# Performance work log

Hardware: AMD Instinct MI355X
Metric: run time of the kernel (lower is better)

## Reference

```python
import jax, jax.numpy as jnp
import numpy as np

B, S, H, A = 64, 4096, 256, 128


def entmax15(z):
    # exact entmax-1.5 along the last axis (Peters & Martins 2019)
    z = z / 2.0
    z = z - jnp.max(z, axis=-1, keepdims=True)
    zs = -jnp.sort(-z, axis=-1)                      # descending sort
    n = zs.shape[-1]
    k = jnp.arange(1, n + 1, dtype=z.dtype)
    mean = jnp.cumsum(zs, axis=-1) / k
    mean_sq = jnp.cumsum(zs * zs, axis=-1) / k
    ss = k * (mean_sq - mean * mean)
    delta = jnp.clip((1.0 - ss) / k, 0.0)
    tau = mean - jnp.sqrt(delta)
    k_star = jnp.sum(tau <= zs, axis=-1)             # support size per row
    tau_star = jnp.take_along_axis(tau, (k_star - 1)[..., None], axis=-1)
    return jnp.square(jnp.clip(z - tau_star, 0.0))


def setup_inputs() -> dict:
    key = jax.random.key(0)
    k0, k1, k2, k3, k4 = jax.random.split(key, 5)
    lim1 = 1.0 / np.sqrt(H)
    lim2 = 1.0 / np.sqrt(A)
    return {
        "lstm_output": jax.random.normal(k0, (B, S, H), dtype=jnp.float32),
        "W1": jax.random.uniform(k1, (H, A), jnp.float32, -lim1, lim1),
        "b1": jax.random.uniform(k2, (A,), jnp.float32, -lim1, lim1),
        "W2": jax.random.uniform(k3, (A, 1), jnp.float32, -lim2, lim2),
        "b2": jax.random.uniform(k4, (1,), jnp.float32, -lim2, lim2),
    }


def reference(lstm_output, W1, b1, W2, b2):
    # score MLP: Linear -> Tanh -> Linear -> squeeze(-1)  => [B, S]
    h = jnp.tanh(jnp.einsum("bsh,ha->bsa", lstm_output, W1) + b1)
    scores = (jnp.einsum("bsa,ao->bso", h, W2) + b2)[..., 0]
    weights = entmax15(scores)                       # entmax over seq axis (dim=1)
    context = jnp.einsum("bsh,bs->bh", lstm_output, weights)
    return (context, weights)
```

## Files before the change

### kernel.cpp

```cpp
#include <hip/hip_runtime.h>
#include <hip/hip_bf16.h>

#define BB 64
#define SS 4096
#define HH 256
#define AA 128
#define MT 128
#define BK 64
#define XST 72

typedef _Float16 half4v __attribute__((ext_vector_type(4)));
typedef _Float16 half8v __attribute__((ext_vector_type(8)));
typedef float floatx16 __attribute__((ext_vector_type(16)));

__device__ __forceinline__ float fast_tanh(float x) {
    float xc = fminf(fmaxf(x, -9.0f), 9.0f);
    float e = __expf(2.0f * xc);
    return 1.0f - __fdividef(2.0f, e + 1.0f);
}

__global__ void convert_w1(const float* __restrict__ W1, _Float16* __restrict__ Wt) {
    int n = blockIdx.x;
    int k = threadIdx.x;
    Wt[n * HH + k] = (_Float16)W1[k * AA + n];
}

__global__ __launch_bounds__(256) void score_mfma(
    const float* __restrict__ X,
    const _Float16* __restrict__ Wt,
    const float* __restrict__ b1,
    const float* __restrict__ W2,
    const float* __restrict__ b2,
    float* __restrict__ scores)
{
    __shared__ float smem_f[9216];
    _Float16* Xs = (_Float16*)smem_f;
    _Float16* Ws = (_Float16*)smem_f + MT * XST;
    float* part = smem_f;

    const int tid   = threadIdx.x;
    const int m0    = blockIdx.x * MT;
    const int wid   = tid >> 6;
    const int lane  = tid & 63;
    const int lrow  = lane & 31;
    const int lhalf = lane >> 5;
    const int wr    = (wid & 1) * 64;
    const int wc    = (wid >> 1) * 64;

    floatx16 acc[2][2];
    #pragma unroll
    for (int i = 0; i < 2; ++i)
        #pragma unroll
        for (int j = 0; j < 2; ++j)
            #pragma unroll
            for (int r = 0; r < 16; ++r) acc[i][j][r] = 0.0f;

    for (int k0 = 0; k0 < HH; k0 += BK) {
        #pragma unroll
        for (int p = 0; p < 8; ++p) {
            int idx = tid + p * 256;
            int row = idx >> 4, c4 = idx & 15;
            float4 v = *(const float4*)(X + (size_t)(m0 + row) * HH + k0 + c4 * 4);
            half4v hv;
            hv[0] = (_Float16)v.x; hv[1] = (_Float16)v.y;
            hv[2] = (_Float16)v.z; hv[3] = (_Float16)v.w;
            *(half4v*)(Xs + row * XST + c4 * 4) = hv;
        }
        #pragma unroll
        for (int p = 0; p < 4; ++p) {
            int idx = tid + p * 256;
            int n = idx >> 3, u = idx & 7;
            uint4 v = *(const uint4*)(Wt + (size_t)n * HH + k0 + u * 8);
            *(uint4*)(Ws + n * XST + u * 8) = v;
        }
        __syncthreads();
        #pragma unroll
        for (int kk = 0; kk < BK; kk += 16) {
            half8v a0 = *(half8v*)(Xs + (wr + lrow) * XST + kk + lhalf * 8);
            half8v a1 = *(half8v*)(Xs + (wr + 32 + lrow) * XST + kk + lhalf * 8);
            half8v b0 = *(half8v*)(Ws + (wc + lrow) * XST + kk + lhalf * 8);
            half8v bq = *(half8v*)(Ws + (wc + 32 + lrow) * XST + kk + lhalf * 8);
            acc[0][0] = __builtin_amdgcn_mfma_f32_32x32x16_f16(a0, b0, acc[0][0], 0, 0, 0);
            acc[0][1] = __builtin_amdgcn_mfma_f32_32x32x16_f16(a0, bq, acc[0][1], 0, 0, 0);
            acc[1][0] = __builtin_amdgcn_mfma_f32_32x32x16_f16(a1, b0, acc[1][0], 0, 0, 0);
            acc[1][1] = __builtin_amdgcn_mfma_f32_32x32x16_f16(a1, bq, acc[1][1], 0, 0, 0);
        }
        __syncthreads();
    }

    const int cA = wc + lrow;
    const int cB = wc + 32 + lrow;
    const float b1A = b1[cA], b1B = b1[cB];
    const float w2A = W2[cA], w2B = W2[cB];
    #pragma unroll
    for (int i = 0; i < 2; ++i) {
        #pragma unroll
        for (int r = 0; r < 16; ++r) {
            float hA = fast_tanh(acc[i][0][r] + b1A) * w2A;
            float hB = fast_tanh(acc[i][1][r] + b1B) * w2B;
            int row = wr + i * 32 + (r & 3) + 8 * (r >> 2) + 4 * lhalf;
            part[row * 65 + (wid >> 1) * 32 + lrow] = hA + hB;
        }
    }
    __syncthreads();
    if (tid < MT) {
        float s = b2[0];
        #pragma unroll
        for (int c = 0; c < 64; ++c) s += part[tid * 65 + c];
        scores[m0 + tid] = s;
    }
}

__global__ __launch_bounds__(256) void entmax_kernel(
    float* __restrict__ buf, float* __restrict__ ctx)
{
    __shared__ float sred[4];
    const int b = blockIdx.x, tid = threadIdx.x;
    float* p = buf + (size_t)b * SS;

    float z[16];
    #pragma unroll
    for (int j = 0; j < 16; ++j) z[j] = p[tid + j * 256] * 0.5f;

    float m = -1e30f;
    #pragma unroll
    for (int j = 0; j < 16; ++j) m = fmaxf(m, z[j]);
    #pragma unroll
    for (int o = 1; o < 64; o <<= 1) m = fmaxf(m, __shfl_xor(m, o));
    if ((tid & 63) == 0) sred[tid >> 6] = m;
    __syncthreads();
    m = fmaxf(fmaxf(sred[0], sred[1]), fmaxf(sred[2], sred[3]));
    __syncthreads();
    #pragma unroll
    for (int j = 0; j < 16; ++j) z[j] -= m;

    float lo = -1.0f, hi = 0.0f;
    for (int it = 0; it < 35; ++it) {
        float tau = 0.5f * (lo + hi);
        float s = 0.0f;
        #pragma unroll
        for (int j = 0; j < 16; ++j) {
            float d = fmaxf(z[j] - tau, 0.0f);
            s = fmaf(d, d, s);
        }
        #pragma unroll
        for (int o = 1; o < 64; o <<= 1) s += __shfl_xor(s, o);
        if ((tid & 63) == 0) sred[tid >> 6] = s;
        __syncthreads();
        s = sred[0] + sred[1] + sred[2] + sred[3];
        __syncthreads();
        if (s >= 1.0f) lo = tau; else hi = tau;
    }
    const float tau = 0.5f * (lo + hi);

    #pragma unroll
    for (int j = 0; j < 16; ++j) {
        float d = fmaxf(z[j] - tau, 0.0f);
        p[tid + j * 256] = d * d;
    }
    ctx[b * HH + tid] = 0.0f;
}

__global__ __launch_bounds__(256) void context_kernel(
    const float* __restrict__ X, const float* __restrict__ w,
    float* __restrict__ ctx)
{
    const int b  = blockIdx.y;
    const int s0 = blockIdx.x * 128;
    const int h  = threadIdx.x;

    __shared__ float ws_[128];
    __shared__ int nzflag;
    if (h == 0) nzflag = 0;
    __syncthreads();
    if (h < 128) {
        float v = w[(size_t)b * SS + s0 + h];
        ws_[h] = v;
        if (v > 0.0f) nzflag = 1;
    }
    __syncthreads();
    if (!nzflag) return;

    float acc = 0.0f;
    const float* xp = X + ((size_t)b * SS + s0) * HH + h;
    #pragma unroll 4
    for (int i = 0; i < 128; ++i) {
        float wv = ws_[i];
        if (wv != 0.0f) acc = fmaf(xp[(size_t)i * HH], wv, acc);
    }
    atomicAdd(&ctx[b * HH + h], acc);
}

extern "C" void kernel_launch(void* const* d_in, const int* in_sizes, int n_in,
                              void* d_out, int out_size, void* d_ws, size_t ws_size,
                              hipStream_t stream) {
    const float* X  = (const float*)d_in[0];
    const float* W1 = (const float*)d_in[1];
    const float* b1 = (const float*)d_in[2];
    const float* W2 = (const float*)d_in[3];
    const float* b2 = (const float*)d_in[4];

    float* out = (float*)d_out;
    float* ctx = out;
    float* wts = out + BB * HH;
    _Float16* Wt = (_Float16*)d_ws;

    convert_w1<<<AA, HH, 0, stream>>>(W1, Wt);
    score_mfma<<<(BB * SS) / MT, 256, 0, stream>>>(X, Wt, b1, W2, b2, wts);
    entmax_kernel<<<BB, 256, 0, stream>>>(wts, ctx);
    context_kernel<<<dim3(SS / 128, BB), 256, 0, stream>>>(X, wts, ctx);
}
```

Measured before the change: 401.4 us.

## Stream X directly into MFMA registers without LDS staging per wave

The score GEMM no longer stages X and W tiles in shared memory behind block barriers. Each wave now owns 32 rows and the full 128-column output, loading X rows straight from global memory into fp16 MFMA operands and reading W fragments from global memory (L2/L1 cached). The second linear layer is reduced with wave shuffles instead of an LDS partial-sum buffer. This removes the LDS traffic and __syncthreads, at the cost of repeated, uncoalesced global loads of W per wave and less load coalescing for X.

```diff
diff --git a/kernel.cpp b/kernel.cpp
--- a/kernel.cpp
+++ b/kernel.cpp
@@ -5,11 +5,7 @@
 #define SS 4096
 #define HH 256
 #define AA 128
-#define MT 128
-#define BK 64
-#define XST 72
 
-typedef _Float16 half4v __attribute__((ext_vector_type(4)));
 typedef _Float16 half8v __attribute__((ext_vector_type(8)));
 typedef float floatx16 __attribute__((ext_vector_type(16)));
 
@@ -25,7 +21,7 @@
     Wt[n * HH + k] = (_Float16)W1[k * AA + n];
 }
 
-__global__ __launch_bounds__(256) void score_mfma(
+__global__ __launch_bounds__(256) void score_stream(
     const float* __restrict__ X,
     const _Float16* __restrict__ Wt,
     const float* __restrict__ b1,
@@ -33,81 +29,59 @@
     const float* __restrict__ b2,
     float* __restrict__ scores)
 {
-    __shared__ float smem_f[9216];
-    _Float16* Xs = (_Float16*)smem_f;
-    _Float16* Ws = (_Float16*)smem_f + MT * XST;
-    float* part = smem_f;
-
     const int tid   = threadIdx.x;
-    const int m0    = blockIdx.x * MT;
     const int wid   = tid >> 6;
     const int lane  = tid & 63;
     const int lrow  = lane & 31;
     const int lhalf = lane >> 5;
-    const int wr    = (wid & 1) * 64;
-    const int wc    = (wid >> 1) * 64;
+    const int m0    = blockIdx.x * 128 + wid * 32;
 
-    floatx16 acc[2][2];
+    const float* xp = X + (size_t)(m0 + lrow) * HH + lhalf * 8;
+
+    floatx16 acc[4];
     #pragma unroll
-    for (int i = 0; i < 2; ++i)
+    for (int nt = 0; nt < 4; ++nt)
         #pragma unroll
-        for (int j = 0; j < 2; ++j)
-            #pragma unroll
-            for (int r = 0; r < 16; ++r) acc[i][j][r] = 0.0f;
+        for (int r = 0; r < 16; ++r) acc[nt][r] = 0.0f;
 
-    for (int k0 = 0; k0 < HH; k0 += BK) {
+    #pragma unroll
+    for (int kk = 0; kk < 16; ++kk) {
+        float4 v0 = *(const float4*)(xp + kk * 16);
+        float4 v1 = *(const float4*)(xp + kk * 16 + 4);
+        half8v a;
+        a[0] = (_Float16)v0.x; a[1] = (_Float16)v0.y;
+        a[2] = (_Float16)v0.z; a[3] = (_Float16)v0.w;
+        a[4] = (_Float16)v1.x; a[5] = (_Float16)v1.y;
+        a[6] = (_Float16)v1.z; a[7] = (_Float16)v1.w;
         #pragma unroll
-        for (int p = 0; p < 8; ++p) {
-            int idx = tid + p * 256;
-            int row = idx >> 4, c4 = idx & 15;
-            float4 v = *(const float4*)(X + (size_t)(m0 + row) * HH + k0 + c4 * 4);
-            half4v hv;
-            hv[0] = (_Float16)v.x; hv[1] = (_Float16)v.y;
-            hv[2] = (_Float16)v.z; hv[3] = (_Float16)v.w;
-            *(half4v*)(Xs + row * XST + c4 * 4) = hv;
+        for (int nt = 0; nt < 4; ++nt) {
+            half8v b = *(const half8v*)(Wt + (size_t)(nt * 32 + lrow) * HH
+                                        + kk * 16 + lhalf * 8);
+            acc[nt] = __builtin_amdgcn_mfma_f32_32x32x16_f16(a, b, acc[nt], 0, 0, 0);
         }
-        #pragma unroll
-        for (int p = 0; p < 4; ++p) {
-            int idx = tid + p * 256;
-            int n = idx >> 3, u = idx & 7;
-            uint4 v = *(const uint4*)(Wt + (size_t)n * HH + k0 + u * 8);
-            *(uint4*)(Ws + n * XST + u * 8) = v;
-        }
-        __syncthreads();
-        #pragma unroll
-        for (int kk = 0; kk < BK; kk += 16) {
-            half8v a0 = *(half8v*)(Xs + (wr + lrow) * XST + kk + lhalf * 8);
-            half8v a1 = *(half8v*)(Xs + (wr + 32 + lrow) * XST + kk + lhalf * 8);
-            half8v b0 = *(half8v*)(Ws + (wc + lrow) * XST + kk + lhalf * 8);
-            half8v bq = *(half8v*)(Ws + (wc + 32 + lrow) * XST + kk + lhalf * 8);
-            acc[0][0] = __builtin_amdgcn_mfma_f32_32x32x16_f16(a0, b0, acc[0][0], 0, 0, 0);
-            acc[0][1] = __builtin_amdgcn_mfma_f32_32x32x16_f16(a0, bq, acc[0][1], 0, 0, 0);
-            acc[1][0] = __builtin_amdgcn_mfma_f32_32x32x16_f16(a1, b0, acc[1][0], 0, 0, 0);
-            acc[1][1] = __builtin_amdgcn_mfma_f32_32x32x16_f16(a1, bq, acc[1][1], 0, 0, 0);
-        }
-        __syncthreads();
     }
 
-    const int cA = wc + lrow;
-    const int cB = wc + 32 + lrow;
-    const float b1A = b1[cA], b1B = b1[cB];
-    const float w2A = W2[cA], w2B = W2[cB];
+    float cb1[4], cw2[4];
     #pragma unroll
-    for (int i = 0; i < 2; ++i) {
+    for (int nt = 0; nt < 4; ++nt) {
+        int col = nt * 32 + lrow;
+        cb1[nt] = b1[col];
+        cw2[nt] = W2[col];
+    }
+    const float bias2 = b2[0];
+
+    #pragma unroll
+    for (int r = 0; r < 16; ++r) {
+        float s = 0.0f;
         #pragma unroll
-        for (int r = 0; r < 16; ++r) {
-            float hA = fast_tanh(acc[i][0][r] + b1A) * w2A;
-            float hB = fast_tanh(acc[i][1][r] + b1B) * w2B;
-            int row = wr + i * 32 + (r & 3) + 8 * (r >> 2) + 4 * lhalf;
-            part[row * 65 + (wid >> 1) * 32 + lrow] = hA + hB;
+        for (int nt = 0; nt < 4; ++nt)
+            s += fast_tanh(acc[nt][r] + cb1[nt]) * cw2[nt];
+        #pragma unroll
+        for (int o = 1; o < 32; o <<= 1) s += __shfl_xor(s, o);
+        if (lrow == 0) {
+            int rr = (r & 3) + 8 * (r >> 2) + 4 * lhalf;
+            scores[m0 + rr] = s + bias2;
         }
-    }
-    __syncthreads();
-    if (tid < MT) {
-        float s = b2[0];
-        #pragma unroll
-        for (int c = 0; c < 64; ++c) s += part[tid * 65 + c];
-        scores[m0 + tid] = s;
     }
 }
 
@@ -206,7 +180,7 @@
     _Float16* Wt = (_Float16*)d_ws;
 
     convert_w1<<<AA, HH, 0, stream>>>(W1, Wt);
-    score_mfma<<<(BB * SS) / MT, 256, 0, stream>>>(X, Wt, b1, W2, b2, wts);
+    score_stream<<<(BB * SS) / 128, 256, 0, stream>>>(X, Wt, b1, W2, b2, wts);
     entmax_kernel<<<BB, 256, 0, stream>>>(wts, ctx);
     context_kernel<<<dim3(SS / 128, BB), 256, 0, stream>>>(X, wts, ctx);
 }
```

After: 453.2 us. 12.9% more time.
